# Kernel optimization log

Measured on AMD Instinct MI355X. Metric: run time of the kernel, lower is better.

Reference implementation:

```python
import jax, jax.numpy as jnp
import numpy as np

NEG_SLOPE = 0.1


def setup_inputs() -> dict:
    key = jax.random.key(0)
    ks = jax.random.split(key, 6)
    B, S, D = 512, 256, 256
    x = jax.random.normal(ks[0], (B, S, D), dtype=jnp.float32)
    pos_matrix = jax.random.normal(ks[1], (B, S, S, 1), dtype=jnp.float32)
    # fc1: Linear(D, D)
    W1 = jax.random.normal(ks[2], (D, D), dtype=jnp.float32) * (1.0 / np.sqrt(D))
    b1 = jax.random.normal(ks[3], (D,), dtype=jnp.float32) * 0.02
    # attn_fc: Linear(2D, 1) -> weight (2D,), bias scalar
    a_w = jax.random.normal(ks[4], (2 * D,), dtype=jnp.float32) * (1.0 / np.sqrt(2 * D))
    a_b = jax.random.normal(ks[5], (1,), dtype=jnp.float32) * 0.02
    return {"x": x, "pos_matrix": pos_matrix, "W1": W1, "b1": b1, "a_w": a_w, "a_b": a_b}


def reference(x, pos_matrix, W1, b1, a_w, a_b):
    # x: (B, S, D); Wh[b,i] = fc1(x[b,i])
    Wh = jnp.einsum("bsd,ed->bse", x, W1) + b1  # (B, S, D)
    D = Wh.shape[-1]
    # attn_fc(concat(Wh_i, Wh_j)) = Wh_i @ a_l + Wh_j @ a_r + a_b
    # (identical math to materializing the (B,S,S,2D) concat tensor)
    a_l, a_r = a_w[:D], a_w[D:]
    e_l = Wh @ a_l  # (B, S) contribution of the head (i) node
    e_r = Wh @ a_r  # (B, S) contribution of the end  (j) node
    s = e_l[:, :, None] + e_r[:, None, :] + a_b[0]  # (B, S, S)
    s = jnp.where(s >= 0, s, NEG_SLOPE * s)  # LeakyReLU(0.1)
    s = s[..., None] + pos_matrix  # (B, S, S, 1)
    w = jax.nn.softmax(s, axis=2)[..., 0]  # softmax over j -> (B, S, S)
    # output[b,i] = ELU( sum_j w[b,i,j] * Wh[b,j] )
    agg = jnp.einsum("bij,bjd->bid", w, Wh)  # (B, S, D)
    return jax.nn.elu(agg)
```

## Files before the change

### kernel.cpp

```cpp
#include <hip/hip_runtime.h>
#include <math.h>

#define NEG_SLOPE 0.1f

constexpr int Bn = 512;
constexpr int Sn = 256;
constexpr int Dn = 256;
constexpr int Mn = Bn * Sn;

typedef short bf16x8 __attribute__((ext_vector_type(8)));
typedef float f32x4 __attribute__((ext_vector_type(4)));

__device__ inline ushort f2bf(float f) {
  uint u = __float_as_uint(f);
  uint r = u + 0x7FFFu + ((u >> 16) & 1u);
  return (ushort)(r >> 16);
}

__global__ __launch_bounds__(256) void k_prep(const float* __restrict__ w1,
                                              ushort* __restrict__ w1h) {
  int idx = blockIdx.x * 256 + threadIdx.x;
  w1h[idx] = f2bf(w1[idx]);
}

__global__ __launch_bounds__(256) void k_vec(const float* __restrict__ w1,
                                             const float* __restrict__ a_w,
                                             const float* __restrict__ b1,
                                             float* __restrict__ vlr) {
  int d = threadIdx.x;
  int e0 = blockIdx.x * 32;
  float vl = 0.f, vr = 0.f;
  for (int e = e0; e < e0 + 32; ++e) {
    float w = w1[(size_t)e * 256 + d];
    vl += w * a_w[e];
    vr += w * a_w[256 + e];
  }
  atomicAdd(&vlr[d], vl);
  atomicAdd(&vlr[256 + d], vr);
  if (blockIdx.x == 0) {
    float pl = b1[d] * a_w[d], pr = b1[d] * a_w[256 + d];
#pragma unroll
    for (int o = 1; o < 64; o <<= 1) {
      pl += __shfl_xor(pl, o);
      pr += __shfl_xor(pr, o);
    }
    if ((threadIdx.x & 63) == 0) {
      atomicAdd(&vlr[512], pl);
      atomicAdd(&vlr[513], pr);
    }
  }
}

__global__ __launch_bounds__(256) void k_gemm1(const float* __restrict__ x,
                                               const ushort* __restrict__ w1h,
                                               const float* __restrict__ b1,
                                               const float* __restrict__ vlr,
                                               ushort* __restrict__ whT,
                                               float* __restrict__ e_l,
                                               float* __restrict__ e_r) {
  __shared__ __align__(16) ushort smem[256 * 72];
  __shared__ float vl_s[256], vr_s[256];
  ushort* Ah = smem;
  ushort* T = smem;

  const int t = threadIdx.x;
  const int wave = t >> 6, lane = t & 63;
  const int q = lane >> 4, c = lane & 15;
  const int row0 = blockIdx.x * 64;
  const int n0 = wave * 64;

  vl_s[t] = vlr[t];
  vr_s[t] = vlr[256 + t];

  f32x4 acc[4][4];
#pragma unroll
  for (int mi = 0; mi < 4; ++mi)
#pragma unroll
    for (int nt = 0; nt < 4; ++nt) acc[mi][nt] = (f32x4){0.f, 0.f, 0.f, 0.f};

  const int r = t >> 2;
  const int kq = (t & 3) << 4;
  const float* xrow = x + (size_t)(row0 + r) * 256 + kq;
  float sl = 0.f, sr = 0.f;

  for (int k0 = 0; k0 < 256; k0 += 64) {
    float4 v0 = *(const float4*)(xrow + k0 + 0);
    float4 v1 = *(const float4*)(xrow + k0 + 4);
    float4 v2 = *(const float4*)(xrow + k0 + 8);
    float4 v3 = *(const float4*)(xrow + k0 + 12);
    __syncthreads();
    {
      float vv[16] = {v0.x, v0.y, v0.z, v0.w, v1.x, v1.y, v1.z, v1.w,
                      v2.x, v2.y, v2.z, v2.w, v3.x, v3.y, v3.z, v3.w};
#pragma unroll
      for (int j = 0; j < 16; ++j) {
        sl += vv[j] * vl_s[k0 + kq + j];
        sr += vv[j] * vr_s[k0 + kq + j];
      }
#pragma unroll
      for (int j = 0; j < 4; ++j) {
        ushort4 h;
        ushort* hp = (ushort*)&h;
#pragma unroll
        for (int e = 0; e < 4; ++e) hp[e] = f2bf(vv[j * 4 + e]);
        *(ushort4*)&Ah[r * 72 + kq + j * 4] = h;
      }
    }
    __syncthreads();

#pragma unroll
    for (int kk = 0; kk < 64; kk += 32) {
      bf16x8 bh[4];
#pragma unroll
      for (int nt = 0; nt < 4; ++nt)
        bh[nt] = *(const bf16x8*)(w1h + (size_t)(n0 + nt * 16 + c) * 256 + (k0 + kk) + q * 8);
#pragma unroll
      for (int mi = 0; mi < 4; ++mi) {
        bf16x8 ah = *(const bf16x8*)&Ah[(mi * 16 + c) * 72 + kk + q * 8];
#pragma unroll
        for (int nt = 0; nt < 4; ++nt)
          acc[mi][nt] = __builtin_amdgcn_mfma_f32_16x16x32_bf16(ah, bh[nt], acc[mi][nt], 0, 0, 0);
      }
    }
  }

  sl += __shfl_xor(sl, 1); sl += __shfl_xor(sl, 2);
  sr += __shfl_xor(sr, 1); sr += __shfl_xor(sr, 2);
  if ((t & 3) == 0) {
    e_l[row0 + r] = sl + vlr[512];
    e_r[row0 + r] = sr + vlr[513];
  }

  float b1v[4];
#pragma unroll
  for (int nt = 0; nt < 4; ++nt) b1v[nt] = b1[n0 + nt * 16 + c];
  __syncthreads();
#pragma unroll
  for (int mi = 0; mi < 4; ++mi)
#pragma unroll
    for (int nt = 0; nt < 4; ++nt) {
      ushort4 h;
      ushort* hp = (ushort*)&h;
#pragma unroll
      for (int reg = 0; reg < 4; ++reg) hp[reg] = f2bf(acc[mi][nt][reg] + b1v[nt]);
      *(ushort4*)&T[(size_t)(n0 + nt * 16 + c) * 72 + mi * 16 + q * 4] = h;
    }
  __syncthreads();
  {
    const int b = row0 >> 8, s0 = row0 & 255;
    ushort* dst = whT + ((size_t)b * 256 + t) * 256 + s0;
#pragma unroll
    for (int j = 0; j < 8; ++j)
      *(uint4*)(dst + j * 8) = *(const uint4*)&T[t * 72 + j * 8];
  }
}

__global__ __launch_bounds__(256) void k_attn(const ushort* __restrict__ whT,
                                              const float* __restrict__ pos,
                                              const float* __restrict__ e_l,
                                              const float* __restrict__ e_r,
                                              const float* __restrict__ a_b,
                                              float* __restrict__ out) {
  __shared__ __align__(16) ushort ph[64 * 264];
  __shared__ __align__(16) float er_s[256];
  __shared__ float el_s[64];
  __shared__ float rsum[64];

  const int t = threadIdx.x;
  const int wave = t >> 6, lane = t & 63;
  const int q = lane >> 4, c = lane & 15;
  const int b = blockIdx.y, i0 = blockIdx.x * 64;

  er_s[t] = e_r[b * 256 + t];
  if (t < 64) el_s[t] = e_l[b * 256 + i0 + t];
  __syncthreads();

  const float ab = a_b[0];
  const float* posb = pos + ((size_t)b * 256 + i0) * 256;
#pragma unroll 4
  for (int ii = 0; ii < 16; ++ii) {
    int i = ii * 4 + wave;
    float4 pv = *(const float4*)(posb + (size_t)i * 256 + lane * 4);
    float el = el_s[i];
    float4 er = *(const float4*)&er_s[lane * 4];
    float s0 = el + er.x + ab; s0 = (s0 >= 0.f) ? s0 : NEG_SLOPE * s0; s0 += pv.x;
    float s1 = el + er.y + ab; s1 = (s1 >= 0.f) ? s1 : NEG_SLOPE * s1; s1 += pv.y;
    float s2 = el + er.z + ab; s2 = (s2 >= 0.f) ? s2 : NEG_SLOPE * s2; s2 += pv.z;
    float s3 = el + er.w + ab; s3 = (s3 >= 0.f) ? s3 : NEG_SLOPE * s3; s3 += pv.w;
    float e0 = __expf(s0), e1 = __expf(s1), e2 = __expf(s2), e3 = __expf(s3);
    float rs = e0 + e1 + e2 + e3;
#pragma unroll
    for (int off = 1; off < 64; off <<= 1) rs += __shfl_xor(rs, off);
    ushort4 h;
    ushort* hp = (ushort*)&h;
    hp[0] = f2bf(e0); hp[1] = f2bf(e1); hp[2] = f2bf(e2); hp[3] = f2bf(e3);
    *(ushort4*)&ph[i * 264 + lane * 4] = h;
    if (lane == 0) rsum[i] = rs;
  }
  __syncthreads();

  f32x4 acc[4][4];
#pragma unroll
  for (int mi = 0; mi < 4; ++mi)
#pragma unroll
    for (int nt = 0; nt < 4; ++nt) acc[mi][nt] = (f32x4){0.f, 0.f, 0.f, 0.f};

  const int n0 = wave * 64;
  const ushort* wb = whT + (size_t)b * 65536;
  for (int kk = 0; kk < 256; kk += 32) {
    bf16x8 bfr[4];
#pragma unroll
    for (int nt = 0; nt < 4; ++nt)
      bfr[nt] = *(const bf16x8*)(wb + (size_t)(n0 + nt * 16 + c) * 256 + kk + q * 8);
#pragma unroll
    for (int mi = 0; mi < 4; ++mi) {
      bf16x8 ah = *(const bf16x8*)&ph[(mi * 16 + c) * 264 + kk + q * 8];
#pragma unroll
      for (int nt = 0; nt < 4; ++nt)
        acc[mi][nt] = __builtin_amdgcn_mfma_f32_16x16x32_bf16(ah, bfr[nt], acc[mi][nt], 0, 0, 0);
    }
  }

  float* outb = out + ((size_t)b * 256 + i0) * 256;
#pragma unroll
  for (int mi = 0; mi < 4; ++mi) {
    float alpha[4];
#pragma unroll
    for (int reg = 0; reg < 4; ++reg) alpha[reg] = 1.0f / rsum[mi * 16 + q * 4 + reg];
#pragma unroll
    for (int nt = 0; nt < 4; ++nt)
#pragma unroll
      for (int reg = 0; reg < 4; ++reg) {
        float v = acc[mi][nt][reg] * alpha[reg];
        v = (v > 0.f) ? v : (__expf(v) - 1.0f);
        outb[(size_t)(mi * 16 + q * 4 + reg) * 256 + n0 + nt * 16 + c] = v;
      }
  }
}

extern "C" void kernel_launch(void* const* d_in, const int* in_sizes, int n_in,
                              void* d_out, int out_size, void* d_ws, size_t ws_size,
                              hipStream_t stream) {
  const float* x   = (const float*)d_in[0];
  const float* pos = (const float*)d_in[1];
  const float* w1  = (const float*)d_in[2];
  const float* b1  = (const float*)d_in[3];
  const float* a_w = (const float*)d_in[4];
  const float* a_b = (const float*)d_in[5];
  float* out = (float*)d_out;

  ushort* w1h = (ushort*)d_ws;
  ushort* whT = w1h + 65536;
  float*  e_l = (float*)(whT + (size_t)33554432);
  float*  e_r = e_l + Mn;
  float*  vlr = e_r + Mn;

  hipMemsetAsync(vlr, 0, 514 * sizeof(float), stream);
  k_prep<<<dim3(256), dim3(256), 0, stream>>>(w1, w1h);
  k_vec<<<dim3(8), dim3(256), 0, stream>>>(w1, a_w, b1, vlr);
  k_gemm1<<<dim3(Mn / 64), dim3(256), 0, stream>>>(x, w1h, b1, vlr, whT, e_l, e_r);
  k_attn<<<dim3(Sn / 64, Bn), dim3(256), 0, stream>>>(whT, pos, e_l, e_r, a_b, out);
}
```

Before: 412.5 us.

## Pipeline attention softmax and aggregation over 64-column chunks with double-buffered LDS

```diff
diff --git a/kernel.cpp b/kernel.cpp
--- a/kernel.cpp
+++ b/kernel.cpp
@@ -161,7 +161,7 @@
                                               const float* __restrict__ e_r,
                                               const float* __restrict__ a_b,
                                               float* __restrict__ out) {
-  __shared__ __align__(16) ushort ph[64 * 264];
+  __shared__ __align__(16) ushort ph[2][64 * 72];
   __shared__ __align__(16) float er_s[256];
   __shared__ float el_s[64];
   __shared__ float rsum[64];
@@ -173,53 +173,87 @@
 
   er_s[t] = e_r[b * 256 + t];
   if (t < 64) el_s[t] = e_l[b * 256 + i0 + t];
-  __syncthreads();
-
+
+  const int r16 = wave * 16;
   const float ab = a_b[0];
   const float* posb = pos + ((size_t)b * 256 + i0) * 256;
-#pragma unroll 4
-  for (int ii = 0; ii < 16; ++ii) {
-    int i = ii * 4 + wave;
-    float4 pv = *(const float4*)(posb + (size_t)i * 256 + lane * 4);
-    float el = el_s[i];
-    float4 er = *(const float4*)&er_s[lane * 4];
-    float s0 = el + er.x + ab; s0 = (s0 >= 0.f) ? s0 : NEG_SLOPE * s0; s0 += pv.x;
-    float s1 = el + er.y + ab; s1 = (s1 >= 0.f) ? s1 : NEG_SLOPE * s1; s1 += pv.y;
-    float s2 = el + er.z + ab; s2 = (s2 >= 0.f) ? s2 : NEG_SLOPE * s2; s2 += pv.z;
-    float s3 = el + er.w + ab; s3 = (s3 >= 0.f) ? s3 : NEG_SLOPE * s3; s3 += pv.w;
-    float e0 = __expf(s0), e1 = __expf(s1), e2 = __expf(s2), e3 = __expf(s3);
-    float rs = e0 + e1 + e2 + e3;
-#pragma unroll
-    for (int off = 1; off < 64; off <<= 1) rs += __shfl_xor(rs, off);
-    ushort4 h;
-    ushort* hp = (ushort*)&h;
-    hp[0] = f2bf(e0); hp[1] = f2bf(e1); hp[2] = f2bf(e2); hp[3] = f2bf(e3);
-    *(ushort4*)&ph[i * 264 + lane * 4] = h;
-    if (lane == 0) rsum[i] = rs;
-  }
-  __syncthreads();
 
   f32x4 acc[4][4];
 #pragma unroll
   for (int mi = 0; mi < 4; ++mi)
 #pragma unroll
     for (int nt = 0; nt < 4; ++nt) acc[mi][nt] = (f32x4){0.f, 0.f, 0.f, 0.f};
+
+  float psum[4] = {0.f, 0.f, 0.f, 0.f};
+
+  float4 pv[4];
+#pragma unroll
+  for (int it = 0; it < 4; ++it)
+    pv[it] = *(const float4*)(posb + (size_t)(r16 + it * 4 + q) * 256 + c * 4);
+
+  __syncthreads();
 
   const int n0 = wave * 64;
   const ushort* wb = whT + (size_t)b * 65536;
-  for (int kk = 0; kk < 256; kk += 32) {
-    bf16x8 bfr[4];
-#pragma unroll
-    for (int nt = 0; nt < 4; ++nt)
-      bfr[nt] = *(const bf16x8*)(wb + (size_t)(n0 + nt * 16 + c) * 256 + kk + q * 8);
-#pragma unroll
-    for (int mi = 0; mi < 4; ++mi) {
-      bf16x8 ah = *(const bf16x8*)&ph[(mi * 16 + c) * 264 + kk + q * 8];
+
+  for (int tc = 0; tc < 4; ++tc) {
+    const int j0 = tc * 64;
+    ushort* phb = &ph[tc & 1][0];
+
+    float4 pn[4];
+    if (tc < 3) {
+#pragma unroll
+      for (int it = 0; it < 4; ++it)
+        pn[it] = *(const float4*)(posb + (size_t)(r16 + it * 4 + q) * 256 + j0 + 64 + c * 4);
+    }
+
+    float4 er = *(const float4*)&er_s[j0 + c * 4];
+#pragma unroll
+    for (int it = 0; it < 4; ++it) {
+      const int row = r16 + it * 4 + q;
+      const float el = el_s[row];
+      float s0 = el + er.x + ab; s0 = (s0 >= 0.f) ? s0 : NEG_SLOPE * s0; s0 += pv[it].x;
+      float s1 = el + er.y + ab; s1 = (s1 >= 0.f) ? s1 : NEG_SLOPE * s1; s1 += pv[it].y;
+      float s2 = el + er.z + ab; s2 = (s2 >= 0.f) ? s2 : NEG_SLOPE * s2; s2 += pv[it].z;
+      float s3 = el + er.w + ab; s3 = (s3 >= 0.f) ? s3 : NEG_SLOPE * s3; s3 += pv[it].w;
+      float e0 = __expf(s0), e1 = __expf(s1), e2 = __expf(s2), e3 = __expf(s3);
+      psum[it] += e0 + e1 + e2 + e3;
+      ushort4 h;
+      ushort* hp = (ushort*)&h;
+      hp[0] = f2bf(e0); hp[1] = f2bf(e1); hp[2] = f2bf(e2); hp[3] = f2bf(e3);
+      *(ushort4*)&phb[row * 72 + c * 4] = h;
+    }
+    __syncthreads();
+
+#pragma unroll
+    for (int kk = 0; kk < 64; kk += 32) {
+      bf16x8 bfr[4];
 #pragma unroll
       for (int nt = 0; nt < 4; ++nt)
-        acc[mi][nt] = __builtin_amdgcn_mfma_f32_16x16x32_bf16(ah, bfr[nt], acc[mi][nt], 0, 0, 0);
-    }
-  }
+        bfr[nt] = *(const bf16x8*)(wb + (size_t)(n0 + nt * 16 + c) * 256 + j0 + kk + q * 8);
+#pragma unroll
+      for (int mi = 0; mi < 4; ++mi) {
+        bf16x8 ah = *(const bf16x8*)&phb[(mi * 16 + c) * 72 + kk + q * 8];
+#pragma unroll
+        for (int nt = 0; nt < 4; ++nt)
+          acc[mi][nt] = __builtin_amdgcn_mfma_f32_16x16x32_bf16(ah, bfr[nt], acc[mi][nt], 0, 0, 0);
+      }
+    }
+
+#pragma unroll
+    for (int it = 0; it < 4; ++it) pv[it] = pn[it];
+  }
+
+#pragma unroll
+  for (int it = 0; it < 4; ++it) {
+    float p = psum[it];
+    p += __shfl_xor(p, 1);
+    p += __shfl_xor(p, 2);
+    p += __shfl_xor(p, 4);
+    p += __shfl_xor(p, 8);
+    if (c == 0) rsum[r16 + it * 4 + q] = p;
+  }
+  __syncthreads();
 
   float* outb = out + ((size_t)b * 256 + i0) * 256;
 #pragma unroll
```

New measurement: 399.4 us. 3.2% less time.

## Fuse fc1 GEMM and attention into one per-batch kernel with LDS-resident Wh

Applied to the files above, without the earlier changes.

```diff
diff --git a/kernel.cpp b/kernel.cpp
--- a/kernel.cpp
+++ b/kernel.cpp
@@ -6,7 +6,6 @@
 constexpr int Bn = 512;
 constexpr int Sn = 256;
 constexpr int Dn = 256;
-constexpr int Mn = Bn * Sn;
 
 typedef short bf16x8 __attribute__((ext_vector_type(8)));
 typedef float f32x4 __attribute__((ext_vector_type(4)));
@@ -17,224 +16,263 @@
   return (ushort)(r >> 16);
 }
 
-__global__ __launch_bounds__(256) void k_prep(const float* __restrict__ w1,
-                                              ushort* __restrict__ w1h) {
+#define BAR() asm volatile("s_waitcnt lgkmcnt(0)\n\ts_barrier" ::: "memory")
+
+__global__ __launch_bounds__(256) void k_prep_vec(const float* __restrict__ w1,
+                                                  const float* __restrict__ a_w,
+                                                  const float* __restrict__ b1,
+                                                  ushort* __restrict__ w1h,
+                                                  float* __restrict__ vlr) {
   int idx = blockIdx.x * 256 + threadIdx.x;
   w1h[idx] = f2bf(w1[idx]);
-}
-
-__global__ __launch_bounds__(256) void k_vec(const float* __restrict__ w1,
-                                             const float* __restrict__ a_w,
-                                             const float* __restrict__ b1,
-                                             float* __restrict__ vlr) {
-  int d = threadIdx.x;
-  int e0 = blockIdx.x * 32;
-  float vl = 0.f, vr = 0.f;
-  for (int e = e0; e < e0 + 32; ++e) {
-    float w = w1[(size_t)e * 256 + d];
-    vl += w * a_w[e];
-    vr += w * a_w[256 + e];
-  }
-  atomicAdd(&vlr[d], vl);
-  atomicAdd(&vlr[256 + d], vr);
-  if (blockIdx.x == 0) {
-    float pl = b1[d] * a_w[d], pr = b1[d] * a_w[256 + d];
-#pragma unroll
-    for (int o = 1; o < 64; o <<= 1) {
-      pl += __shfl_xor(pl, o);
-      pr += __shfl_xor(pr, o);
-    }
-    if ((threadIdx.x & 63) == 0) {
-      atomicAdd(&vlr[512], pl);
-      atomicAdd(&vlr[513], pr);
-    }
-  }
-}
-
-__global__ __launch_bounds__(256) void k_gemm1(const float* __restrict__ x,
+  if (blockIdx.x < 8) {
+    int d = threadIdx.x;
+    int e0 = blockIdx.x * 32;
+    float vl = 0.f, vr = 0.f;
+    for (int e = e0; e < e0 + 32; ++e) {
+      float w = w1[(size_t)e * 256 + d];
+      vl += w * a_w[e];
+      vr += w * a_w[256 + e];
+    }
+    atomicAdd(&vlr[d], vl);
+    atomicAdd(&vlr[256 + d], vr);
+    if (blockIdx.x == 0) {
+      float pl = b1[d] * a_w[d], pr = b1[d] * a_w[256 + d];
+#pragma unroll
+      for (int o = 1; o < 64; o <<= 1) {
+        pl += __shfl_xor(pl, o);
+        pr += __shfl_xor(pr, o);
+      }
+      if ((threadIdx.x & 63) == 0) {
+        atomicAdd(&vlr[512], pl);
+        atomicAdd(&vlr[513], pr);
+      }
+    }
+  }
+}
+
+__global__ __launch_bounds__(512) void k_fused(const float* __restrict__ x,
                                                const ushort* __restrict__ w1h,
                                                const float* __restrict__ b1,
                                                const float* __restrict__ vlr,
-                                               ushort* __restrict__ whT,
-                                               float* __restrict__ e_l,
-                                               float* __restrict__ e_r) {
-  __shared__ __align__(16) ushort smem[256 * 72];
-  __shared__ float vl_s[256], vr_s[256];
-  ushort* Ah = smem;
-  ushort* T = smem;
+                                               const float* __restrict__ pos,
+                                               const float* __restrict__ a_b,
+                                               float* __restrict__ out) {
+  __shared__ __align__(16) ushort WhT_s[65536];
+  __shared__ __align__(16) ushort AhPh[9216];
+  __shared__ __align__(16) float vl_s[256];
+  __shared__ __align__(16) float vr_s[256];
+  __shared__ __align__(16) float el_s[256];
+  __shared__ __align__(16) float er_s[256];
+  __shared__ float rsum[64];
 
   const int t = threadIdx.x;
   const int wave = t >> 6, lane = t & 63;
   const int q = lane >> 4, c = lane & 15;
-  const int row0 = blockIdx.x * 64;
-  const int n0 = wave * 64;
-
-  vl_s[t] = vlr[t];
-  vr_s[t] = vlr[256 + t];
-
-  f32x4 acc[4][4];
+  const int b = blockIdx.x;
+
+  const float cl = vlr[512], cr = vlr[513];
+  const float ab = a_b[0];
+
+  if (t < 256) {
+    vl_s[t] = vlr[t];
+    vr_s[t] = vlr[256 + t];
+  }
+
+  const int g = wave >> 2;
+  const int wg = wave & 3;
+  const int n0A = wg * 64;
+  const int tt = t & 255;
+  const int r = tt >> 2;
+  const int kq = (tt & 3) << 4;
+  const float* xb = x + (size_t)b * 65536;
+  ushort* Ahg = AhPh + g * 4608;
+
+  float b1v[4];
+#pragma unroll
+  for (int nt = 0; nt < 4; ++nt) b1v[nt] = b1[n0A + nt * 16 + c];
+
+  {
+    f32x4 acc[4][4];
+#pragma unroll
+    for (int mi = 0; mi < 4; ++mi)
+#pragma unroll
+      for (int nt = 0; nt < 4; ++nt) acc[mi][nt] = (f32x4){0.f, 0.f, 0.f, 0.f};
+    float sl = 0.f, sr = 0.f;
+
+    float4 V0, V1, V2, V3, N0, N1, N2, N3;
+    {
+      const float* p = xb + (size_t)((g * 2) * 64 + r) * 256 + kq;
+      V0 = *(const float4*)(p); V1 = *(const float4*)(p + 4);
+      V2 = *(const float4*)(p + 8); V3 = *(const float4*)(p + 12);
+    }
+
+#pragma unroll
+    for (int sk = 0; sk < 8; ++sk) {
+      const int stile = g * 2 + (sk >> 2);
+      const int k0 = (sk & 3) * 64;
+      if (sk < 7) {
+        const int s2 = g * 2 + ((sk + 1) >> 2), kn = ((sk + 1) & 3) * 64;
+        const float* p = xb + (size_t)(s2 * 64 + r) * 256 + kn + kq;
+        N0 = *(const float4*)(p); N1 = *(const float4*)(p + 4);
+        N2 = *(const float4*)(p + 8); N3 = *(const float4*)(p + 12);
+      }
+      BAR();
+      {
+        float vv[16] = {V0.x, V0.y, V0.z, V0.w, V1.x, V1.y, V1.z, V1.w,
+                        V2.x, V2.y, V2.z, V2.w, V3.x, V3.y, V3.z, V3.w};
+#pragma unroll
+        for (int j = 0; j < 16; ++j) {
+          sl += vv[j] * vl_s[k0 + kq + j];
+          sr += vv[j] * vr_s[k0 + kq + j];
+        }
+#pragma unroll
+        for (int j = 0; j < 4; ++j) {
+          ushort4 h;
+          ushort* hp = (ushort*)&h;
+#pragma unroll
+          for (int e = 0; e < 4; ++e) hp[e] = f2bf(vv[j * 4 + e]);
+          *(ushort4*)&Ahg[r * 72 + kq + j * 4] = h;
+        }
+      }
+      BAR();
+
+#pragma unroll
+      for (int kk = 0; kk < 64; kk += 32) {
+        bf16x8 bh[4];
+#pragma unroll
+        for (int nt = 0; nt < 4; ++nt)
+          bh[nt] = *(const bf16x8*)(w1h + (size_t)(n0A + nt * 16 + c) * 256 + k0 + kk + q * 8);
+#pragma unroll
+        for (int mi = 0; mi < 4; ++mi) {
+          bf16x8 ah = *(const bf16x8*)&Ahg[(mi * 16 + c) * 72 + kk + q * 8];
+#pragma unroll
+          for (int nt = 0; nt < 4; ++nt)
+            acc[mi][nt] = __builtin_amdgcn_mfma_f32_16x16x32_bf16(ah, bh[nt], acc[mi][nt], 0, 0, 0);
+        }
+      }
+
+      if ((sk & 3) == 3) {
+        sl += __shfl_xor(sl, 1); sl += __shfl_xor(sl, 2);
+        sr += __shfl_xor(sr, 1); sr += __shfl_xor(sr, 2);
+        if ((tt & 3) == 0) {
+          el_s[stile * 64 + r] = sl + cl;
+          er_s[stile * 64 + r] = sr + cr;
+        }
+#pragma unroll
+        for (int mi = 0; mi < 4; ++mi)
+#pragma unroll
+          for (int nt = 0; nt < 4; ++nt) {
+            ushort4 h;
+            ushort* hp = (ushort*)&h;
+#pragma unroll
+            for (int reg = 0; reg < 4; ++reg) hp[reg] = f2bf(acc[mi][nt][reg] + b1v[nt]);
+            uint idx = (uint)(n0A + nt * 16 + c) * 256 + stile * 64 + mi * 16 + q * 4;
+            idx ^= (uint)((c & 7) << 3);
+            *(ushort4*)&WhT_s[idx] = h;
+            acc[mi][nt] = (f32x4){0.f, 0.f, 0.f, 0.f};
+          }
+        sl = 0.f; sr = 0.f;
+      }
+      if (sk < 7) { V0 = N0; V1 = N1; V2 = N2; V3 = N3; }
+    }
+  }
+
+  const float* posb = pos + (size_t)b * 65536;
+  float4 Pa0, Pa1, Pb0, Pb1, Pc0, Pc1;
+  {
+    const float* p0 = posb + (size_t)(wave * 8 + q) * 256 + c * 4;
+    Pa0 = *(const float4*)p0; Pa1 = *(const float4*)(p0 + 1024);
+    const float* p1 = posb + (size_t)(wave * 8 + q) * 256 + 64 + c * 4;
+    Pb0 = *(const float4*)p1; Pb1 = *(const float4*)(p1 + 1024);
+  }
+  BAR();
+
+  const int n0B = wave * 32;
+  f32x4 accB[4][2];
 #pragma unroll
   for (int mi = 0; mi < 4; ++mi)
 #pragma unroll
-    for (int nt = 0; nt < 4; ++nt) acc[mi][nt] = (f32x4){0.f, 0.f, 0.f, 0.f};
-
-  const int r = t >> 2;
-  const int kq = (t & 3) << 4;
-  const float* xrow = x + (size_t)(row0 + r) * 256 + kq;
-  float sl = 0.f, sr = 0.f;
-
-  for (int k0 = 0; k0 < 256; k0 += 64) {
-    float4 v0 = *(const float4*)(xrow + k0 + 0);
-    float4 v1 = *(const float4*)(xrow + k0 + 4);
-    float4 v2 = *(const float4*)(xrow + k0 + 8);
-    float4 v3 = *(const float4*)(xrow + k0 + 12);
-    __syncthreads();
-    {
-      float vv[16] = {v0.x, v0.y, v0.z, v0.w, v1.x, v1.y, v1.z, v1.w,
-                      v2.x, v2.y, v2.z, v2.w, v3.x, v3.y, v3.z, v3.w};
-#pragma unroll
-      for (int j = 0; j < 16; ++j) {
-        sl += vv[j] * vl_s[k0 + kq + j];
-        sr += vv[j] * vr_s[k0 + kq + j];
-      }
-#pragma unroll
-      for (int j = 0; j < 4; ++j) {
-        ushort4 h;
-        ushort* hp = (ushort*)&h;
-#pragma unroll
-        for (int e = 0; e < 4; ++e) hp[e] = f2bf(vv[j * 4 + e]);
-        *(ushort4*)&Ah[r * 72 + kq + j * 4] = h;
-      }
-    }
-    __syncthreads();
-
-#pragma unroll
-    for (int kk = 0; kk < 64; kk += 32) {
-      bf16x8 bh[4];
-#pragma unroll
-      for (int nt = 0; nt < 4; ++nt)
-        bh[nt] = *(const bf16x8*)(w1h + (size_t)(n0 + nt * 16 + c) * 256 + (k0 + kk) + q * 8);
-#pragma unroll
-      for (int mi = 0; mi < 4; ++mi) {
-        bf16x8 ah = *(const bf16x8*)&Ah[(mi * 16 + c) * 72 + kk + q * 8];
-#pragma unroll
-        for (int nt = 0; nt < 4; ++nt)
-          acc[mi][nt] = __builtin_amdgcn_mfma_f32_16x16x32_bf16(ah, bh[nt], acc[mi][nt], 0, 0, 0);
-      }
-    }
-  }
-
-  sl += __shfl_xor(sl, 1); sl += __shfl_xor(sl, 2);
-  sr += __shfl_xor(sr, 1); sr += __shfl_xor(sr, 2);
-  if ((t & 3) == 0) {
-    e_l[row0 + r] = sl + vlr[512];
-    e_r[row0 + r] = sr + vlr[513];
-  }
-
-  float b1v[4];
-#pragma unroll
-  for (int nt = 0; nt < 4; ++nt) b1v[nt] = b1[n0 + nt * 16 + c];
-  __syncthreads();
-#pragma unroll
-  for (int mi = 0; mi < 4; ++mi)
-#pragma unroll
-    for (int nt = 0; nt < 4; ++nt) {
+    for (int nt = 0; nt < 2; ++nt) accB[mi][nt] = (f32x4){0.f, 0.f, 0.f, 0.f};
+  float psum0 = 0.f, psum1 = 0.f;
+
+#pragma unroll
+  for (int gc = 0; gc < 16; ++gc) {
+    const int itile = gc >> 2, tc = gc & 3;
+    if (gc < 14) {
+      const int i2 = (gc + 2) >> 2, t2 = (gc + 2) & 3;
+      const float* p = posb + (size_t)(i2 * 64 + wave * 8 + q) * 256 + t2 * 64 + c * 4;
+      Pc0 = *(const float4*)p; Pc1 = *(const float4*)(p + 1024);
+    }
+    ushort* phb = AhPh + (gc & 1) * 4608;
+
+    float4 er = *(const float4*)&er_s[tc * 64 + c * 4];
+#pragma unroll
+    for (int it2 = 0; it2 < 2; ++it2) {
+      const int rl = wave * 8 + it2 * 4 + q;
+      const float el = el_s[itile * 64 + rl];
+      float4 pv = it2 ? Pa1 : Pa0;
+      float s0 = el + er.x + ab; s0 = (s0 >= 0.f) ? s0 : NEG_SLOPE * s0; s0 += pv.x;
+      float s1 = el + er.y + ab; s1 = (s1 >= 0.f) ? s1 : NEG_SLOPE * s1; s1 += pv.y;
+      float s2 = el + er.z + ab; s2 = (s2 >= 0.f) ? s2 : NEG_SLOPE * s2; s2 += pv.z;
+      float s3 = el + er.w + ab; s3 = (s3 >= 0.f) ? s3 : NEG_SLOPE * s3; s3 += pv.w;
+      float e0 = __expf(s0), e1 = __expf(s1), e2 = __expf(s2), e3 = __expf(s3);
+      if (it2) psum1 += e0 + e1 + e2 + e3; else psum0 += e0 + e1 + e2 + e3;
       ushort4 h;
       ushort* hp = (ushort*)&h;
-#pragma unroll
-      for (int reg = 0; reg < 4; ++reg) hp[reg] = f2bf(acc[mi][nt][reg] + b1v[nt]);
-      *(ushort4*)&T[(size_t)(n0 + nt * 16 + c) * 72 + mi * 16 + q * 4] = h;
-    }
-  __syncthreads();
-  {
-    const int b = row0 >> 8, s0 = row0 & 255;
-    ushort* dst = whT + ((size_t)b * 256 + t) * 256 + s0;
-#pragma unroll
-    for (int j = 0; j < 8; ++j)
-      *(uint4*)(dst + j * 8) = *(const uint4*)&T[t * 72 + j * 8];
-  }
-}
-
-__global__ __launch_bounds__(256) void k_attn(const ushort* __restrict__ whT,
-                                              const float* __restrict__ pos,
-                                              const float* __restrict__ e_l,
-                                              const float* __restrict__ e_r,
-                                              const float* __restrict__ a_b,
-                                              float* __restrict__ out) {
-  __shared__ __align__(16) ushort ph[64 * 264];
-  __shared__ __align__(16) float er_s[256];
-  __shared__ float el_s[64];
-  __shared__ float rsum[64];
-
-  const int t = threadIdx.x;
-  const int wave = t >> 6, lane = t & 63;
-  const int q = lane >> 4, c = lane & 15;
-  const int b = blockIdx.y, i0 = blockIdx.x * 64;
-
-  er_s[t] = e_r[b * 256 + t];
-  if (t < 64) el_s[t] = e_l[b * 256 + i0 + t];
-  __syncthreads();
-
-  const float ab = a_b[0];
-  const float* posb = pos + ((size_t)b * 256 + i0) * 256;
-#pragma unroll 4
-  for (int ii = 0; ii < 16; ++ii) {
-    int i = ii * 4 + wave;
-    float4 pv = *(const float4*)(posb + (size_t)i * 256 + lane * 4);
-    float el = el_s[i];
-    float4 er = *(const float4*)&er_s[lane * 4];
-    float s0 = el + er.x + ab; s0 = (s0 >= 0.f) ? s0 : NEG_SLOPE * s0; s0 += pv.x;
-    float s1 = el + er.y + ab; s1 = (s1 >= 0.f) ? s1 : NEG_SLOPE * s1; s1 += pv.y;
-    float s2 = el + er.z + ab; s2 = (s2 >= 0.f) ? s2 : NEG_SLOPE * s2; s2 += pv.z;
-    float s3 = el + er.w + ab; s3 = (s3 >= 0.f) ? s3 : NEG_SLOPE * s3; s3 += pv.w;
-    float e0 = __expf(s0), e1 = __expf(s1), e2 = __expf(s2), e3 = __expf(s3);
-    float rs = e0 + e1 + e2 + e3;
-#pragma unroll
-    for (int off = 1; off < 64; off <<= 1) rs += __shfl_xor(rs, off);
-    ushort4 h;
-    ushort* hp = (ushort*)&h;
-    hp[0] = f2bf(e0); hp[1] = f2bf(e1); hp[2] = f2bf(e2); hp[3] = f2bf(e3);
-    *(ushort4*)&ph[i * 264 + lane * 4] = h;
-    if (lane == 0) rsum[i] = rs;
-  }
-  __syncthreads();
-
-  f32x4 acc[4][4];
-#pragma unroll
-  for (int mi = 0; mi < 4; ++mi)
-#pragma unroll
-    for (int nt = 0; nt < 4; ++nt) acc[mi][nt] = (f32x4){0.f, 0.f, 0.f, 0.f};
-
-  const int n0 = wave * 64;
-  const ushort* wb = whT + (size_t)b * 65536;
-  for (int kk = 0; kk < 256; kk += 32) {
-    bf16x8 bfr[4];
-#pragma unroll
-    for (int nt = 0; nt < 4; ++nt)
-      bfr[nt] = *(const bf16x8*)(wb + (size_t)(n0 + nt * 16 + c) * 256 + kk + q * 8);
-#pragma unroll
-    for (int mi = 0; mi < 4; ++mi) {
-      bf16x8 ah = *(const bf16x8*)&ph[(mi * 16 + c) * 264 + kk + q * 8];
-#pragma unroll
-      for (int nt = 0; nt < 4; ++nt)
-        acc[mi][nt] = __builtin_amdgcn_mfma_f32_16x16x32_bf16(ah, bfr[nt], acc[mi][nt], 0, 0, 0);
-    }
-  }
-
-  float* outb = out + ((size_t)b * 256 + i0) * 256;
-#pragma unroll
-  for (int mi = 0; mi < 4; ++mi) {
-    float alpha[4];
-#pragma unroll
-    for (int reg = 0; reg < 4; ++reg) alpha[reg] = 1.0f / rsum[mi * 16 + q * 4 + reg];
-#pragma unroll
-    for (int nt = 0; nt < 4; ++nt)
-#pragma unroll
-      for (int reg = 0; reg < 4; ++reg) {
-        float v = acc[mi][nt][reg] * alpha[reg];
-        v = (v > 0.f) ? v : (__expf(v) - 1.0f);
-        outb[(size_t)(mi * 16 + q * 4 + reg) * 256 + n0 + nt * 16 + c] = v;
-      }
+      hp[0] = f2bf(e0); hp[1] = f2bf(e1); hp[2] = f2bf(e2); hp[3] = f2bf(e3);
+      *(ushort4*)&phb[rl * 72 + c * 4] = h;
+    }
+    BAR();
+
+#pragma unroll
+    for (int kk = 0; kk < 64; kk += 32) {
+      bf16x8 bfr[2];
+#pragma unroll
+      for (int nt = 0; nt < 2; ++nt) {
+        uint idx = (uint)(n0B + nt * 16 + c) * 256 + tc * 64 + kk + q * 8;
+        idx ^= (uint)((c & 7) << 3);
+        bfr[nt] = *(const bf16x8*)&WhT_s[idx];
+      }
+#pragma unroll
+      for (int mi = 0; mi < 4; ++mi) {
+        bf16x8 ah = *(const bf16x8*)&phb[(mi * 16 + c) * 72 + kk + q * 8];
+#pragma unroll
+        for (int nt = 0; nt < 2; ++nt)
+          accB[mi][nt] = __builtin_amdgcn_mfma_f32_16x16x32_bf16(ah, bfr[nt], accB[mi][nt], 0, 0, 0);
+      }
+    }
+
+    if (tc == 3) {
+      float p0v = psum0, p1v = psum1;
+      p0v += __shfl_xor(p0v, 1); p0v += __shfl_xor(p0v, 2);
+      p0v += __shfl_xor(p0v, 4); p0v += __shfl_xor(p0v, 8);
+      p1v += __shfl_xor(p1v, 1); p1v += __shfl_xor(p1v, 2);
+      p1v += __shfl_xor(p1v, 4); p1v += __shfl_xor(p1v, 8);
+      if (c == 0) {
+        rsum[wave * 8 + q] = p0v;
+        rsum[wave * 8 + 4 + q] = p1v;
+      }
+      psum0 = 0.f; psum1 = 0.f;
+      BAR();
+      float* outb = out + ((size_t)b * 256 + itile * 64) * 256;
+#pragma unroll
+      for (int mi = 0; mi < 4; ++mi) {
+        float alpha[4];
+#pragma unroll
+        for (int reg = 0; reg < 4; ++reg) alpha[reg] = 1.0f / rsum[mi * 16 + q * 4 + reg];
+#pragma unroll
+        for (int nt = 0; nt < 2; ++nt)
+#pragma unroll
+          for (int reg = 0; reg < 4; ++reg) {
+            float v = accB[mi][nt][reg] * alpha[reg];
+            v = (v > 0.f) ? v : (__expf(v) - 1.0f);
+            outb[(size_t)(mi * 16 + q * 4 + reg) * 256 + n0B + nt * 16 + c] = v;
+            accB[mi][nt][reg] = 0.f;
+          }
+      }
+    }
+    Pa0 = Pb0; Pa1 = Pb1; Pb0 = Pc0; Pb1 = Pc1;
   }
 }
 
@@ -250,14 +288,9 @@
   float* out = (float*)d_out;
 
   ushort* w1h = (ushort*)d_ws;
-  ushort* whT = w1h + 65536;
-  float*  e_l = (float*)(whT + (size_t)33554432);
-  float*  e_r = e_l + Mn;
-  float*  vlr = e_r + Mn;
+  float*  vlr = (float*)(w1h + 65536);
 
   hipMemsetAsync(vlr, 0, 514 * sizeof(float), stream);
-  k_prep<<<dim3(256), dim3(256), 0, stream>>>(w1, w1h);
-  k_vec<<<dim3(8), dim3(256), 0, stream>>>(w1, a_w, b1, vlr);
-  k_gemm1<<<dim3(Mn / 64), dim3(256), 0, stream>>>(x, w1h, b1, vlr, whT, e_l, e_r);
-  k_attn<<<dim3(Sn / 64, Bn), dim3(256), 0, stream>>>(whT, pos, e_l, e_r, a_b, out);
-}
+  k_prep_vec<<<dim3(256), dim3(256), 0, stream>>>(w1, a_w, b1, w1h, vlr);
+  k_fused<<<dim3(Bn), dim3(512), 0, stream>>>(x, w1h, b1, vlr, pos, a_b, out);
+}
```

Measured after the change: 347.9 us. 1.19x faster.

## Fuse all stages into one per-batch kernel with Wh kept in LDS

Applied to the files above, without the earlier changes.

```diff
diff --git a/kernel.cpp b/kernel.cpp
--- a/kernel.cpp
+++ b/kernel.cpp
@@ -6,7 +6,6 @@
 constexpr int Bn = 512;
 constexpr int Sn = 256;
 constexpr int Dn = 256;
-constexpr int Mn = Bn * Sn;
 
 typedef short bf16x8 __attribute__((ext_vector_type(8)));
 typedef float f32x4 __attribute__((ext_vector_type(4)));
@@ -17,124 +16,128 @@
   return (ushort)(r >> 16);
 }
 
-__global__ __launch_bounds__(256) void k_prep(const float* __restrict__ w1,
-                                              ushort* __restrict__ w1h) {
-  int idx = blockIdx.x * 256 + threadIdx.x;
-  w1h[idx] = f2bf(w1[idx]);
-}
-
-__global__ __launch_bounds__(256) void k_vec(const float* __restrict__ w1,
-                                             const float* __restrict__ a_w,
-                                             const float* __restrict__ b1,
-                                             float* __restrict__ vlr) {
-  int d = threadIdx.x;
-  int e0 = blockIdx.x * 32;
-  float vl = 0.f, vr = 0.f;
-  for (int e = e0; e < e0 + 32; ++e) {
-    float w = w1[(size_t)e * 256 + d];
-    vl += w * a_w[e];
-    vr += w * a_w[256 + e];
-  }
-  atomicAdd(&vlr[d], vl);
-  atomicAdd(&vlr[256 + d], vr);
-  if (blockIdx.x == 0) {
-    float pl = b1[d] * a_w[d], pr = b1[d] * a_w[256 + d];
+#define BAR() asm volatile("s_waitcnt lgkmcnt(0)\n\ts_barrier" ::: "memory")
+
+__global__ __launch_bounds__(1024) void k_all(const float* __restrict__ x,
+                                              const float* __restrict__ pos,
+                                              const float* __restrict__ w1,
+                                              const float* __restrict__ b1,
+                                              const float* __restrict__ a_w,
+                                              const float* __restrict__ a_b,
+                                              float* __restrict__ out) {
+  __shared__ __align__(16) ushort WhT_s[65536];
+  __shared__ __align__(16) float scr[2048];
+  __shared__ __align__(16) float vl_s[256];
+  __shared__ __align__(16) float vr_s[256];
+  __shared__ __align__(16) float el_s[256];
+  __shared__ __align__(16) float er_s[256];
+  __shared__ float clp[8];
+
+  const int t = threadIdx.x;
+  const int wave = t >> 6, lane = t & 63;
+  const int q = lane >> 4, c = lane & 15;
+  const int b = blockIdx.x;
+
+  {
+    const int d = t & 255, seg = t >> 8;
+    float vl = 0.f, vr = 0.f;
+    const float* wp = w1 + (size_t)(seg * 64) * 256 + d;
+    const float* awl = a_w + seg * 64;
+    const float* awr = a_w + 256 + seg * 64;
+#pragma unroll 8
+    for (int e = 0; e < 64; ++e) {
+      float w = wp[(size_t)e * 256];
+      vl += w * awl[e];
+      vr += w * awr[e];
+    }
+    scr[seg * 256 + d] = vl;
+    scr[1024 + seg * 256 + d] = vr;
+  }
+  __syncthreads();
+  if (t < 256) {
+    vl_s[t] = scr[t] + scr[256 + t] + scr[512 + t] + scr[768 + t];
+    vr_s[t] = scr[1024 + t] + scr[1280 + t] + scr[1536 + t] + scr[1792 + t];
+    float pl = b1[t] * a_w[t], pr = b1[t] * a_w[256 + t];
 #pragma unroll
     for (int o = 1; o < 64; o <<= 1) {
       pl += __shfl_xor(pl, o);
       pr += __shfl_xor(pr, o);
     }
-    if ((threadIdx.x & 63) == 0) {
-      atomicAdd(&vlr[512], pl);
-      atomicAdd(&vlr[513], pr);
-    }
-  }
-}
-
-__global__ __launch_bounds__(256) void k_gemm1(const float* __restrict__ x,
-                                               const ushort* __restrict__ w1h,
-                                               const float* __restrict__ b1,
-                                               const float* __restrict__ vlr,
-                                               ushort* __restrict__ whT,
-                                               float* __restrict__ e_l,
-                                               float* __restrict__ e_r) {
-  __shared__ __align__(16) ushort smem[256 * 72];
-  __shared__ float vl_s[256], vr_s[256];
-  ushort* Ah = smem;
-  ushort* T = smem;
-
-  const int t = threadIdx.x;
-  const int wave = t >> 6, lane = t & 63;
-  const int q = lane >> 4, c = lane & 15;
-  const int row0 = blockIdx.x * 64;
-  const int n0 = wave * 64;
-
-  vl_s[t] = vlr[t];
-  vr_s[t] = vlr[256 + t];
+    if (lane == 0) { clp[wave] = pl; clp[4 + wave] = pr; }
+  }
+  __syncthreads();
+  const float cl = clp[0] + clp[1] + clp[2] + clp[3];
+  const float cr = clp[4] + clp[5] + clp[6] + clp[7];
+  const float ab = a_b[0];
+
+  const int g = wave >> 2, wg = wave & 3;
+  const int n0A = wg * 64;
 
   f32x4 acc[4][4];
 #pragma unroll
   for (int mi = 0; mi < 4; ++mi)
 #pragma unroll
     for (int nt = 0; nt < 4; ++nt) acc[mi][nt] = (f32x4){0.f, 0.f, 0.f, 0.f};
-
-  const int r = t >> 2;
-  const int kq = (t & 3) << 4;
-  const float* xrow = x + (size_t)(row0 + r) * 256 + kq;
-  float sl = 0.f, sr = 0.f;
-
-  for (int k0 = 0; k0 < 256; k0 += 64) {
-    float4 v0 = *(const float4*)(xrow + k0 + 0);
-    float4 v1 = *(const float4*)(xrow + k0 + 4);
-    float4 v2 = *(const float4*)(xrow + k0 + 8);
-    float4 v3 = *(const float4*)(xrow + k0 + 12);
-    __syncthreads();
+  float slm[4] = {0.f, 0.f, 0.f, 0.f}, srm[4] = {0.f, 0.f, 0.f, 0.f};
+  float b1v[4];
+#pragma unroll
+  for (int nt = 0; nt < 4; ++nt) b1v[nt] = b1[n0A + nt * 16 + c];
+
+  const float* xg = x + (size_t)b * 65536 + (size_t)(g * 64 + c) * 256 + q * 8;
+  const float* w1g = w1 + (size_t)(n0A + c) * 256 + q * 8;
+
+#pragma unroll
+  for (int st = 0; st < 8; ++st) {
+    const int k0 = st * 32;
+    bf16x8 ah[4];
     {
-      float vv[16] = {v0.x, v0.y, v0.z, v0.w, v1.x, v1.y, v1.z, v1.w,
-                      v2.x, v2.y, v2.z, v2.w, v3.x, v3.y, v3.z, v3.w};
-#pragma unroll
-      for (int j = 0; j < 16; ++j) {
-        sl += vv[j] * vl_s[k0 + kq + j];
-        sr += vv[j] * vr_s[k0 + kq + j];
+      float4 vla = *(const float4*)&vl_s[k0 + q * 8];
+      float4 vlb = *(const float4*)&vl_s[k0 + q * 8 + 4];
+      float4 vra = *(const float4*)&vr_s[k0 + q * 8];
+      float4 vrb = *(const float4*)&vr_s[k0 + q * 8 + 4];
+#pragma unroll
+      for (int mi = 0; mi < 4; ++mi) {
+        const float* p = xg + mi * 16 * 256 + k0;
+        float4 xa = *(const float4*)p;
+        float4 xc = *(const float4*)(p + 4);
+        slm[mi] += xa.x * vla.x + xa.y * vla.y + xa.z * vla.z + xa.w * vla.w +
+                   xc.x * vlb.x + xc.y * vlb.y + xc.z * vlb.z + xc.w * vlb.w;
+        srm[mi] += xa.x * vra.x + xa.y * vra.y + xa.z * vra.z + xa.w * vra.w +
+                   xc.x * vrb.x + xc.y * vrb.y + xc.z * vrb.z + xc.w * vrb.w;
+        union { bf16x8 v; ushort u[8]; } ua;
+        ua.u[0] = f2bf(xa.x); ua.u[1] = f2bf(xa.y);
+        ua.u[2] = f2bf(xa.z); ua.u[3] = f2bf(xa.w);
+        ua.u[4] = f2bf(xc.x); ua.u[5] = f2bf(xc.y);
+        ua.u[6] = f2bf(xc.z); ua.u[7] = f2bf(xc.w);
+        ah[mi] = ua.v;
       }
-#pragma unroll
-      for (int j = 0; j < 4; ++j) {
-        ushort4 h;
-        ushort* hp = (ushort*)&h;
-#pragma unroll
-        for (int e = 0; e < 4; ++e) hp[e] = f2bf(vv[j * 4 + e]);
-        *(ushort4*)&Ah[r * 72 + kq + j * 4] = h;
-      }
-    }
-    __syncthreads();
-
-#pragma unroll
-    for (int kk = 0; kk < 64; kk += 32) {
-      bf16x8 bh[4];
-#pragma unroll
-      for (int nt = 0; nt < 4; ++nt)
-        bh[nt] = *(const bf16x8*)(w1h + (size_t)(n0 + nt * 16 + c) * 256 + (k0 + kk) + q * 8);
-#pragma unroll
-      for (int mi = 0; mi < 4; ++mi) {
-        bf16x8 ah = *(const bf16x8*)&Ah[(mi * 16 + c) * 72 + kk + q * 8];
-#pragma unroll
-        for (int nt = 0; nt < 4; ++nt)
-          acc[mi][nt] = __builtin_amdgcn_mfma_f32_16x16x32_bf16(ah, bh[nt], acc[mi][nt], 0, 0, 0);
-      }
-    }
-  }
-
-  sl += __shfl_xor(sl, 1); sl += __shfl_xor(sl, 2);
-  sr += __shfl_xor(sr, 1); sr += __shfl_xor(sr, 2);
-  if ((t & 3) == 0) {
-    e_l[row0 + r] = sl + vlr[512];
-    e_r[row0 + r] = sr + vlr[513];
-  }
-
-  float b1v[4];
-#pragma unroll
-  for (int nt = 0; nt < 4; ++nt) b1v[nt] = b1[n0 + nt * 16 + c];
-  __syncthreads();
+    }
+#pragma unroll
+    for (int nt = 0; nt < 4; ++nt) {
+      const float* p = w1g + nt * 16 * 256 + k0;
+      float4 wa = *(const float4*)p;
+      float4 wc = *(const float4*)(p + 4);
+      union { bf16x8 v; ushort u[8]; } ub;
+      ub.u[0] = f2bf(wa.x); ub.u[1] = f2bf(wa.y);
+      ub.u[2] = f2bf(wa.z); ub.u[3] = f2bf(wa.w);
+      ub.u[4] = f2bf(wc.x); ub.u[5] = f2bf(wc.y);
+      ub.u[6] = f2bf(wc.z); ub.u[7] = f2bf(wc.w);
+#pragma unroll
+      for (int mi = 0; mi < 4; ++mi)
+        acc[mi][nt] = __builtin_amdgcn_mfma_f32_16x16x32_bf16(ah[mi], ub.v, acc[mi][nt], 0, 0, 0);
+    }
+  }
+
+#pragma unroll
+  for (int mi = 0; mi < 4; ++mi) {
+    float s1 = slm[mi]; s1 += __shfl_xor(s1, 16); s1 += __shfl_xor(s1, 32);
+    float s2 = srm[mi]; s2 += __shfl_xor(s2, 16); s2 += __shfl_xor(s2, 32);
+    if (wg == 0 && q == 0) {
+      el_s[g * 64 + mi * 16 + c] = s1 + cl;
+      er_s[g * 64 + mi * 16 + c] = s2 + cr;
+    }
+  }
+
 #pragma unroll
   for (int mi = 0; mi < 4; ++mi)
 #pragma unroll
@@ -143,99 +146,78 @@
       ushort* hp = (ushort*)&h;
 #pragma unroll
       for (int reg = 0; reg < 4; ++reg) hp[reg] = f2bf(acc[mi][nt][reg] + b1v[nt]);
-      *(ushort4*)&T[(size_t)(n0 + nt * 16 + c) * 72 + mi * 16 + q * 4] = h;
-    }
-  __syncthreads();
-  {
-    const int b = row0 >> 8, s0 = row0 & 255;
-    ushort* dst = whT + ((size_t)b * 256 + t) * 256 + s0;
-#pragma unroll
-    for (int j = 0; j < 8; ++j)
-      *(uint4*)(dst + j * 8) = *(const uint4*)&T[t * 72 + j * 8];
-  }
-}
-
-__global__ __launch_bounds__(256) void k_attn(const ushort* __restrict__ whT,
-                                              const float* __restrict__ pos,
-                                              const float* __restrict__ e_l,
-                                              const float* __restrict__ e_r,
-                                              const float* __restrict__ a_b,
-                                              float* __restrict__ out) {
-  __shared__ __align__(16) ushort ph[64 * 264];
-  __shared__ __align__(16) float er_s[256];
-  __shared__ float el_s[64];
-  __shared__ float rsum[64];
-
-  const int t = threadIdx.x;
-  const int wave = t >> 6, lane = t & 63;
-  const int q = lane >> 4, c = lane & 15;
-  const int b = blockIdx.y, i0 = blockIdx.x * 64;
-
-  er_s[t] = e_r[b * 256 + t];
-  if (t < 64) el_s[t] = e_l[b * 256 + i0 + t];
-  __syncthreads();
-
-  const float ab = a_b[0];
-  const float* posb = pos + ((size_t)b * 256 + i0) * 256;
-#pragma unroll 4
-  for (int ii = 0; ii < 16; ++ii) {
-    int i = ii * 4 + wave;
-    float4 pv = *(const float4*)(posb + (size_t)i * 256 + lane * 4);
-    float el = el_s[i];
-    float4 er = *(const float4*)&er_s[lane * 4];
-    float s0 = el + er.x + ab; s0 = (s0 >= 0.f) ? s0 : NEG_SLOPE * s0; s0 += pv.x;
-    float s1 = el + er.y + ab; s1 = (s1 >= 0.f) ? s1 : NEG_SLOPE * s1; s1 += pv.y;
-    float s2 = el + er.z + ab; s2 = (s2 >= 0.f) ? s2 : NEG_SLOPE * s2; s2 += pv.z;
-    float s3 = el + er.w + ab; s3 = (s3 >= 0.f) ? s3 : NEG_SLOPE * s3; s3 += pv.w;
-    float e0 = __expf(s0), e1 = __expf(s1), e2 = __expf(s2), e3 = __expf(s3);
-    float rs = e0 + e1 + e2 + e3;
-#pragma unroll
-    for (int off = 1; off < 64; off <<= 1) rs += __shfl_xor(rs, off);
-    ushort4 h;
-    ushort* hp = (ushort*)&h;
-    hp[0] = f2bf(e0); hp[1] = f2bf(e1); hp[2] = f2bf(e2); hp[3] = f2bf(e3);
-    *(ushort4*)&ph[i * 264 + lane * 4] = h;
-    if (lane == 0) rsum[i] = rs;
-  }
-  __syncthreads();
-
-  f32x4 acc[4][4];
-#pragma unroll
-  for (int mi = 0; mi < 4; ++mi)
-#pragma unroll
-    for (int nt = 0; nt < 4; ++nt) acc[mi][nt] = (f32x4){0.f, 0.f, 0.f, 0.f};
-
-  const int n0 = wave * 64;
-  const ushort* wb = whT + (size_t)b * 65536;
-  for (int kk = 0; kk < 256; kk += 32) {
-    bf16x8 bfr[4];
-#pragma unroll
-    for (int nt = 0; nt < 4; ++nt)
-      bfr[nt] = *(const bf16x8*)(wb + (size_t)(n0 + nt * 16 + c) * 256 + kk + q * 8);
-#pragma unroll
-    for (int mi = 0; mi < 4; ++mi) {
-      bf16x8 ah = *(const bf16x8*)&ph[(mi * 16 + c) * 264 + kk + q * 8];
-#pragma unroll
-      for (int nt = 0; nt < 4; ++nt)
-        acc[mi][nt] = __builtin_amdgcn_mfma_f32_16x16x32_bf16(ah, bfr[nt], acc[mi][nt], 0, 0, 0);
-    }
-  }
-
-  float* outb = out + ((size_t)b * 256 + i0) * 256;
-#pragma unroll
-  for (int mi = 0; mi < 4; ++mi) {
-    float alpha[4];
-#pragma unroll
-    for (int reg = 0; reg < 4; ++reg) alpha[reg] = 1.0f / rsum[mi * 16 + q * 4 + reg];
-#pragma unroll
-    for (int nt = 0; nt < 4; ++nt)
-#pragma unroll
-      for (int reg = 0; reg < 4; ++reg) {
-        float v = acc[mi][nt][reg] * alpha[reg];
-        v = (v > 0.f) ? v : (__expf(v) - 1.0f);
-        outb[(size_t)(mi * 16 + q * 4 + reg) * 256 + n0 + nt * 16 + c] = v;
-      }
-  }
+      uint idx = (uint)(n0A + nt * 16 + c) * 256 + (uint)(g * 64 + mi * 16 + q * 4);
+      idx ^= (uint)((c & 7) << 3);
+      *(ushort4*)&WhT_s[idx] = h;
+    }
+
+  const int rowbase = wave * 16;
+  const float* posr = pos + ((size_t)b * 256 + rowbase + c) * 256 + q * 8;
+  float4 P00 = *(const float4*)posr;
+  float4 P01 = *(const float4*)(posr + 4);
+  float4 P10 = *(const float4*)(posr + 32);
+  float4 P11 = *(const float4*)(posr + 36);
+
+  BAR();
+
+  const float el_c = el_s[rowbase + c];
+  f32x4 aB[16];
+#pragma unroll
+  for (int nt = 0; nt < 16; ++nt) aB[nt] = (f32x4){0.f, 0.f, 0.f, 0.f};
+  float psum = 0.f;
+
+#pragma unroll
+  for (int ch = 0; ch < 8; ++ch) {
+    const int jk = ch * 32;
+    float4 PN0, PN1;
+    if (ch < 6) {
+      PN0 = *(const float4*)(posr + jk + 64);
+      PN1 = *(const float4*)(posr + jk + 68);
+    }
+    float4 er0 = *(const float4*)&er_s[jk + q * 8];
+    float4 er1 = *(const float4*)&er_s[jk + q * 8 + 4];
+    float ev[8];
+    {
+      float s;
+      s = el_c + er0.x + ab; s = (s >= 0.f) ? s : NEG_SLOPE * s; s += P00.x; ev[0] = __expf(s);
+      s = el_c + er0.y + ab; s = (s >= 0.f) ? s : NEG_SLOPE * s; s += P00.y; ev[1] = __expf(s);
+      s = el_c + er0.z + ab; s = (s >= 0.f) ? s : NEG_SLOPE * s; s += P00.z; ev[2] = __expf(s);
+      s = el_c + er0.w + ab; s = (s >= 0.f) ? s : NEG_SLOPE * s; s += P00.w; ev[3] = __expf(s);
+      s = el_c + er1.x + ab; s = (s >= 0.f) ? s : NEG_SLOPE * s; s += P01.x; ev[4] = __expf(s);
+      s = el_c + er1.y + ab; s = (s >= 0.f) ? s : NEG_SLOPE * s; s += P01.y; ev[5] = __expf(s);
+      s = el_c + er1.z + ab; s = (s >= 0.f) ? s : NEG_SLOPE * s; s += P01.z; ev[6] = __expf(s);
+      s = el_c + er1.w + ab; s = (s >= 0.f) ? s : NEG_SLOPE * s; s += P01.w; ev[7] = __expf(s);
+    }
+    psum += ev[0] + ev[1] + ev[2] + ev[3] + ev[4] + ev[5] + ev[6] + ev[7];
+    union { bf16x8 v; ushort u[8]; } up;
+    up.u[0] = f2bf(ev[0]); up.u[1] = f2bf(ev[1]);
+    up.u[2] = f2bf(ev[2]); up.u[3] = f2bf(ev[3]);
+    up.u[4] = f2bf(ev[4]); up.u[5] = f2bf(ev[5]);
+    up.u[6] = f2bf(ev[6]); up.u[7] = f2bf(ev[7]);
+#pragma unroll
+    for (int nt = 0; nt < 16; ++nt) {
+      uint idx = ((uint)(nt * 16 + c) * 256 + (uint)(jk + q * 8)) ^ (uint)((c & 7) << 3);
+      bf16x8 bfr = *(const bf16x8*)&WhT_s[idx];
+      aB[nt] = __builtin_amdgcn_mfma_f32_16x16x32_bf16(up.v, bfr, aB[nt], 0, 0, 0);
+    }
+    P00 = P10; P01 = P11; P10 = PN0; P11 = PN1;
+  }
+
+  psum += __shfl_xor(psum, 16);
+  psum += __shfl_xor(psum, 32);
+  float alpha[4];
+#pragma unroll
+  for (int reg = 0; reg < 4; ++reg) alpha[reg] = 1.0f / __shfl(psum, q * 4 + reg);
+
+  float* outb = out + ((size_t)b * 256 + rowbase) * 256;
+#pragma unroll
+  for (int nt = 0; nt < 16; ++nt)
+#pragma unroll
+    for (int reg = 0; reg < 4; ++reg) {
+      float v = aB[nt][reg] * alpha[reg];
+      v = (v > 0.f) ? v : (__expf(v) - 1.0f);
+      outb[(size_t)(q * 4 + reg) * 256 + nt * 16 + c] = v;
+    }
 }
 
 extern "C" void kernel_launch(void* const* d_in, const int* in_sizes, int n_in,
@@ -249,15 +231,5 @@
   const float* a_b = (const float*)d_in[5];
   float* out = (float*)d_out;
 
-  ushort* w1h = (ushort*)d_ws;
-  ushort* whT = w1h + 65536;
-  float*  e_l = (float*)(whT + (size_t)33554432);
-  float*  e_r = e_l + Mn;
-  float*  vlr = e_r + Mn;
-
-  hipMemsetAsync(vlr, 0, 514 * sizeof(float), stream);
-  k_prep<<<dim3(256), dim3(256), 0, stream>>>(w1, w1h);
-  k_vec<<<dim3(8), dim3(256), 0, stream>>>(w1, a_w, b1, vlr);
-  k_gemm1<<<dim3(Mn / 64), dim3(256), 0, stream>>>(x, w1h, b1, vlr, whT, e_l, e_r);
-  k_attn<<<dim3(Sn / 64, Bn), dim3(256), 0, stream>>>(whT, pos, e_l, e_r, a_b, out);
+  k_all<<<dim3(Bn), dim3(1024), 0, stream>>>(x, pos, w1, b1, a_w, a_b, out);
 }
```

New measurement: 795.6 us. +92.9%, slower.
